# Performance work log

Hardware: AMD Instinct MI355X
Metric: run time of the kernel (lower is better)

The kernel has to match this reference:

```python
import jax, jax.numpy as jnp
import numpy as np

B, R, A, L, P = 1024, 512, 196, 2, 4  # batch, rnn_size, att_size, num_layers, num_parallels


def setup_inputs() -> dict:
    key = jax.random.key(0)
    ks = jax.random.split(key, 24)
    s = 0.02
    inp = {
        'x': jax.random.normal(ks[0], (B, R), jnp.float32),
        'att': jax.random.normal(ks[1], (B, A, R), jnp.float32),
        'inputs': jax.random.normal(ks[2], (2 * L, B, R), jnp.float32),
        # first attention block
        'Wa2a': jax.random.normal(ks[3], (A, R), jnp.float32) * s,
        'ba2a': jnp.zeros((A,), jnp.float32),
        'Wh2a': jax.random.normal(ks[4], (A, R), jnp.float32) * s,
        'bh2a': jnp.zeros((A,), jnp.float32),
        'Wd2d': jax.random.normal(ks[5], (1, A), jnp.float32) * s,
        'bd2d': jnp.zeros((1,), jnp.float32),
        # second attention block
        'Wa2a1': jax.random.normal(ks[6], (A, R), jnp.float32) * s,
        'ba2a1': jnp.zeros((A,), jnp.float32),
        'Wh2a1': jax.random.normal(ks[7], (A, R), jnp.float32) * s,
        'bh2a1': jnp.zeros((A,), jnp.float32),
        'Wd2d1': jax.random.normal(ks[8], (1, A), jnp.float32) * s,
        'bd2d1': jnp.zeros((1,), jnp.float32),
        # per-parallel LSTM gate linears, stacked over P
        'Wi2h': jax.random.normal(ks[9], (P, 4 * R, R), jnp.float32) * s,
        'bi2h': jnp.zeros((P, 4 * R), jnp.float32),
        'Wh2h': jax.random.normal(ks[10], (P, 4 * R, R), jnp.float32) * s,
        'bh2h': jnp.zeros((P, 4 * R), jnp.float32),
        'Wa2h': jax.random.normal(ks[11], (P, 4 * R, R), jnp.float32) * s,
        'ba2h': jnp.zeros((P, 4 * R), jnp.float32),
    }
    return inp


def _attend(att, h, Wa, ba, Wh, bh, Wd, bd):
    # att: [B, S, R] with S == A (code requires it); h: [B, R]
    av = jnp.einsum('bsr,ar->bsa', att, Wa) + ba            # [B, S, A]
    ah = h @ Wh.T + bh                                      # [B, A]
    # original expands h-projection along the LAST axis (unsqueeze(2).expand)
    dot = jnp.tanh(av + ah[:, :, None])                     # [B, S, A]
    score = jnp.einsum('bsa,a->bs', dot, Wd[0]) + bd[0]     # [B, S]
    w = jax.nn.softmax(score, axis=-1)
    return jnp.einsum('bsr,bs->br', att, w)                 # [B, R]


def reference(x, att, inputs, Wa2a, ba2a, Wh2a, bh2a, Wd2d, bd2d,
              Wa2a1, ba2a1, Wh2a1, bh2a1, Wd2d1, bd2d1,
              Wi2h, bi2h, Wh2h, bh2h, Wa2h, ba2h):
    R_ = x.shape[-1]
    L_ = inputs.shape[0] // 2
    outputs = []
    for i in range(L_):
        prev_c = inputs[2 * i]
        prev_h = inputs[2 * i + 1]
        xt = x if i == 0 else x + outputs[-1]
        att_res = _attend(att, prev_h, Wa2a, ba2a, Wh2a, bh2a, Wd2d, bd2d)
        # stacked per-parallel gate sums: [P, B, 4R]
        sums = (jnp.einsum('bd,pgd->pbg', xt, Wi2h) + bi2h[:, None, :]
                + jnp.einsum('bd,pgd->pbg', prev_h, Wh2h) + bh2h[:, None, :]
                + jnp.einsum('bd,pgd->pbg', att_res, Wa2h) + ba2h[:, None, :])
        ig = jax.nn.sigmoid(sums[..., :R_])
        fg = jax.nn.sigmoid(sums[..., R_:2 * R_])
        og = jax.nn.sigmoid(sums[..., 2 * R_:3 * R_])
        it = jnp.tanh(sums[..., 3 * R_:])
        nc = fg * prev_c[None] + ig * it                    # [P, B, R]
        next_c = nc.mean(axis=0)
        next_h = (og * jnp.tanh(nc)).mean(axis=0)
        att_res1 = _attend(att, next_h, Wa2a1, ba2a1, Wh2a1, bh2a1, Wd2d1, bd2d1)
        top_h = att_res1 + next_h
        outputs.append(next_c)
        outputs.append(top_h)
    return jnp.stack(outputs)  # [2L, B, R]
```

## Files before the change

kernel.cpp:

```cpp
#include <hip/hip_runtime.h>
#include <math.h>

typedef __attribute__((ext_vector_type(8))) unsigned short ushort8_t;
typedef __attribute__((ext_vector_type(8))) short bf16x8;
typedef __attribute__((ext_vector_type(4))) float f32x4;

namespace {

constexpr int Bn = 1024;
constexpr int Rn = 512;
constexpr int An = 196;
constexpr int Gn = 8192;
constexpr int Kcat = 1536;
constexpr int NP = 224;
constexpr long ROWS = (long)Bn * An;

__device__ __forceinline__ float b2f(unsigned short u) {
  union { unsigned int i; float f; } v; v.i = ((unsigned int)u) << 16; return v.f;
}
__device__ __forceinline__ unsigned short f2b(float f) {
  union { float f; unsigned int i; } v; v.f = f;
  unsigned int r = v.i + 0x7fffu + ((v.i >> 16) & 1u);
  return (unsigned short)(r >> 16);
}
__device__ __forceinline__ float sigmf(float x) {
  return __builtin_amdgcn_rcpf(1.f + __expf(-x));
}
__device__ __forceinline__ float tanhf_fast(float x) {
  const float e = __expf(2.f * x);
  return 1.f - 2.f * __builtin_amdgcn_rcpf(e + 1.f);
}

__global__ __launch_bounds__(256)
void f2b_copy(const float* __restrict__ src, unsigned short* __restrict__ dst, long n)
{
  long i = ((long)blockIdx.x * 256 + threadIdx.x) * 8;
  const long stride = (long)gridDim.x * 256 * 8;
  for (; i + 8 <= n; i += stride) {
    float4 a = *(const float4*)(src + i);
    float4 b = *(const float4*)(src + i + 4);
    ushort8_t o;
    o[0] = f2b(a.x); o[1] = f2b(a.y); o[2] = f2b(a.z); o[3] = f2b(a.w);
    o[4] = f2b(b.x); o[5] = f2b(b.y); o[6] = f2b(b.z); o[7] = f2b(b.w);
    *(ushort8_t*)(dst + i) = o;
  }
}

__global__ __launch_bounds__(256)
void pack_wpad(const float* __restrict__ Wa0, const float* __restrict__ Wa1,
               unsigned short* __restrict__ Wp)
{
  long i = ((long)blockIdx.x * 256 + threadIdx.x) * 8;
  if (i >= 2L * NP * 512) return;
  const int set = (int)(i / (NP * 512));
  const int rem = (int)(i % (NP * 512));
  const int row = rem / 512, k = rem % 512;
  ushort8_t o;
  if (row < An) {
    const float* s = (set ? Wa1 : Wa0) + (long)row * 512 + k;
    float4 a = *(const float4*)s, b = *(const float4*)(s + 4);
    o[0] = f2b(a.x); o[1] = f2b(a.y); o[2] = f2b(a.z); o[3] = f2b(a.w);
    o[4] = f2b(b.x); o[5] = f2b(b.y); o[6] = f2b(b.z); o[7] = f2b(b.w);
  } else {
    o = ushort8_t{0,0,0,0,0,0,0,0};
  }
  *(ushort8_t*)(Wp + i) = o;
}

__global__ __launch_bounds__(256)
void pack_w(const float* __restrict__ Wi, const float* __restrict__ Wh,
            const float* __restrict__ Wa, unsigned short* __restrict__ W2)
{
  long i = ((long)blockIdx.x * 256 + threadIdx.x) * 8;
  if (i >= (long)Gn * Kcat) return;
  const int g = (int)(i / Kcat);
  const int k = (int)(i % Kcat);
  const float* src = (k < 512) ? Wi + (long)g * 512 + k
                   : (k < 1024) ? Wh + (long)g * 512 + (k - 512)
                   : Wa + (long)g * 512 + (k - 1024);
  float4 a = *(const float4*)src;
  float4 b = *(const float4*)(src + 4);
  ushort8_t o;
  o[0] = f2b(a.x); o[1] = f2b(a.y); o[2] = f2b(a.z); o[3] = f2b(a.w);
  o[4] = f2b(b.x); o[5] = f2b(b.y); o[6] = f2b(b.z); o[7] = f2b(b.w);
  *(ushort8_t*)(W2 + i) = o;
}

__global__ __launch_bounds__(256)
void pack_x(const float* __restrict__ xa, const float* __restrict__ xb,
            const float* __restrict__ h, const float* __restrict__ a,
            unsigned short* __restrict__ X2)
{
  long i = ((long)blockIdx.x * 256 + threadIdx.x) * 8;
  if (i >= (long)Bn * Kcat) return;
  const int b = (int)(i / Kcat);
  const int k = (int)(i % Kcat);
  ushort8_t o;
  if (k < 512) {
    const float* s = xa + (long)b * 512 + k;
    float4 v0 = *(const float4*)s, v1 = *(const float4*)(s + 4);
    if (xb) {
      const float* s2 = xb + (long)b * 512 + k;
      float4 w0 = *(const float4*)s2, w1 = *(const float4*)(s2 + 4);
      v0.x += w0.x; v0.y += w0.y; v0.z += w0.z; v0.w += w0.w;
      v1.x += w1.x; v1.y += w1.y; v1.z += w1.z; v1.w += w1.w;
    }
    o[0] = f2b(v0.x); o[1] = f2b(v0.y); o[2] = f2b(v0.z); o[3] = f2b(v0.w);
    o[4] = f2b(v1.x); o[5] = f2b(v1.y); o[6] = f2b(v1.z); o[7] = f2b(v1.w);
  } else {
    const float* s = (k < 1024) ? h + (long)b * 512 + (k - 512)
                                : a + (long)b * 512 + (k - 1024);
    float4 v0 = *(const float4*)s, v1 = *(const float4*)(s + 4);
    o[0] = f2b(v0.x); o[1] = f2b(v0.y); o[2] = f2b(v0.z); o[3] = f2b(v0.w);
    o[4] = f2b(v1.x); o[5] = f2b(v1.y); o[6] = f2b(v1.z); o[7] = f2b(v1.w);
  }
  *(ushort8_t*)(X2 + i) = o;
}

__global__ __launch_bounds__(512, 4)
void av_cs(const unsigned short* __restrict__ A,
           const unsigned short* __restrict__ Wpad,
           const float* __restrict__ b0vec, const float* __restrict__ b1vec,
           const float* __restrict__ Wd,
           const float* __restrict__ ah0, const float* __restrict__ ah1,
           float* __restrict__ s0, float* __restrict__ s1,
           unsigned short* __restrict__ av_out)
{
  __shared__ unsigned short As[128 * 32];
  __shared__ unsigned short Bs[224 * 32];
  __shared__ float wds[NP], bas[NP];
  __shared__ float ahAs[128], ahBs[128];
  __shared__ float sbA[128], sbB[128];

  const int tid = threadIdx.x;
  const int lane = tid & 63, w = tid >> 6;
  const int wr = w >> 1, wc = w & 1;
  const int fr = lane & 15, q = lane >> 4;
  const long row0 = (long)blockIdx.x * 128;
  const int set = blockIdx.y;

  if (set == 0) {
    if (tid < NP) {
      wds[tid] = (tid < An) ? Wd[tid] : 0.f;
      bas[tid] = (tid < An) ? b0vec[tid] : 0.f;
    }
    if (tid >= 256 && tid < 384) ahAs[tid - 256] = ah0[row0 + tid - 256];
    if (tid >= 384)              ahBs[tid - 384] = ah1[row0 + tid - 384];
  } else {
    if (tid < NP) bas[tid] = (tid < An) ? b1vec[tid] : 0.f;
  }

  const unsigned short* Ab = A + row0 * 512;
  const unsigned short* Bb = Wpad + (long)set * NP * 512;

  f32x4 acc[2][7] = {};

  const int grow = lane >> 2;
  const int gchk = (lane & 3) * 8;

  for (int kt = 0; kt < 512; kt += 32) {
    {
      const unsigned short* src = Ab + (long)(w * 16 + grow) * 512 + gchk + kt;
      __builtin_amdgcn_global_load_lds(
          (const __attribute__((address_space(1))) unsigned int*)src,
          (__attribute__((address_space(3))) unsigned int*)(As + w * 512), 16, 0, 0);
    }
    {
      const unsigned short* src = Bb + (long)(w * 16 + grow) * 512 + gchk + kt;
      __builtin_amdgcn_global_load_lds(
          (const __attribute__((address_space(1))) unsigned int*)src,
          (__attribute__((address_space(3))) unsigned int*)(Bs + w * 512), 16, 0, 0);
    }
    if (w < 6) {
      const unsigned short* src = Bb + (long)((w + 8) * 16 + grow) * 512 + gchk + kt;
      __builtin_amdgcn_global_load_lds(
          (const __attribute__((address_space(1))) unsigned int*)src,
          (__attribute__((address_space(3))) unsigned int*)(Bs + (w + 8) * 512), 16, 0, 0);
    }
    __syncthreads();
    bf16x8 af[2], bfr[7];
#pragma unroll
    for (int m = 0; m < 2; ++m)
      af[m] = *(const bf16x8*)&As[(wr * 32 + m * 16 + fr) * 32 + q * 8];
#pragma unroll
    for (int n = 0; n < 7; ++n)
      bfr[n] = *(const bf16x8*)&Bs[(wc * 112 + n * 16 + fr) * 32 + q * 8];
#pragma unroll
    for (int m = 0; m < 2; ++m)
#pragma unroll
      for (int n = 0; n < 7; ++n)
        acc[m][n] = __builtin_amdgcn_mfma_f32_16x16x32_bf16(af[m], bfr[n], acc[m][n], 0, 0, 0);
    __syncthreads();
  }

  if (set == 0) {
    float pA[2][4], pB[2][4];
#pragma unroll
    for (int m = 0; m < 2; ++m)
#pragma unroll
      for (int j = 0; j < 4; ++j) { pA[m][j] = 0.f; pB[m][j] = 0.f; }
#pragma unroll
    for (int n = 0; n < 7; ++n) {
      const int col = wc * 112 + n * 16 + fr;
      const float wd = wds[col];
      const float bv = bas[col];
#pragma unroll
      for (int m = 0; m < 2; ++m) {
#pragma unroll
        for (int j = 0; j < 4; ++j) {
          const int rl = wr * 32 + m * 16 + q * 4 + j;
          const float av = acc[m][n][j] + bv;
          pA[m][j] += wd * tanhf_fast(av + ahAs[rl]);
          pB[m][j] += wd * tanhf_fast(av + ahBs[rl]);
        }
      }
    }
#pragma unroll
    for (int m = 0; m < 2; ++m)
#pragma unroll
      for (int j = 0; j < 4; ++j) {
#pragma unroll
        for (int off = 1; off < 16; off <<= 1) {
          pA[m][j] += __shfl_xor(pA[m][j], off);
          pB[m][j] += __shfl_xor(pB[m][j], off);
        }
      }
    __syncthreads();
    if (wc == 0 && fr == 0) {
#pragma unroll
      for (int m = 0; m < 2; ++m)
#pragma unroll
        for (int j = 0; j < 4; ++j) {
          const int rl = wr * 32 + m * 16 + q * 4 + j;
          sbA[rl] = pA[m][j]; sbB[rl] = pB[m][j];
        }
    }
    __syncthreads();
    if (wc == 1 && fr == 0) {
#pragma unroll
      for (int m = 0; m < 2; ++m)
#pragma unroll
        for (int j = 0; j < 4; ++j) {
          const int rl = wr * 32 + m * 16 + q * 4 + j;
          sbA[rl] += pA[m][j]; sbB[rl] += pB[m][j];
        }
    }
    __syncthreads();
    if (tid < 128) {
      s0[row0 + tid] = sbA[tid];
      s1[row0 + tid] = sbB[tid];
    }
  } else {
#pragma unroll
    for (int n = 0; n < 7; ++n) {
      const int col = wc * 112 + n * 16 + fr;
      if (col >= An) continue;
      const float bv = bas[col];
#pragma unroll
      for (int m = 0; m < 2; ++m) {
#pragma unroll
        for (int j = 0; j < 4; ++j) {
          const long row = row0 + wr * 32 + m * 16 + q * 4 + j;
          av_out[row * An + col] = f2b(acc[m][n][j] + bv);
        }
      }
    }
  }
}

__global__ __launch_bounds__(256)
void gemm_gate(const unsigned short* __restrict__ A, const unsigned short* __restrict__ Bm,
               const float* __restrict__ bias, float* __restrict__ C)
{
  __shared__ unsigned short As[128 * 32];
  __shared__ unsigned short Bs[128 * 32];
  const int tid = threadIdx.x;
  const int lane = tid & 63, w = tid >> 6;
  int bid = blockIdx.x;
  bid = (bid & 7) * (gridDim.x >> 3) + (bid >> 3);
  const int bx = bid & 63;
  const int by = bid >> 6;
  const long row0 = (long)by * 128;
  const long col0 = (long)bx * 128;
  const int wr = w >> 1, wc = w & 1;
  const int fr = lane & 15, q = lane >> 4;
  const int srow = lane >> 2, schk = lane & 3;

  f32x4 acc[4][4] = {};
  const unsigned short* A0 = A + row0 * Kcat + schk * 8;
  const unsigned short* B0 = Bm + col0 * Kcat + schk * 8;

  for (int kt = 0; kt < Kcat; kt += 32) {
#pragma unroll
    for (int i = 0; i < 2; ++i) {
      const int rr = (w * 2 + i) * 16 + srow;
      __builtin_amdgcn_global_load_lds(
          (const __attribute__((address_space(1))) unsigned int*)(A0 + (long)rr * Kcat + kt),
          (__attribute__((address_space(3))) unsigned int*)(As + (w * 2 + i) * 512),
          16, 0, 0);
      __builtin_amdgcn_global_load_lds(
          (const __attribute__((address_space(1))) unsigned int*)(B0 + (long)rr * Kcat + kt),
          (__attribute__((address_space(3))) unsigned int*)(Bs + (w * 2 + i) * 512),
          16, 0, 0);
    }
    __syncthreads();
    bf16x8 af[4], bfr[4];
#pragma unroll
    for (int m = 0; m < 4; ++m)
      af[m] = *(const bf16x8*)&As[(wr * 64 + m * 16 + fr) * 32 + q * 8];
#pragma unroll
    for (int n = 0; n < 4; ++n)
      bfr[n] = *(const bf16x8*)&Bs[(wc * 64 + n * 16 + fr) * 32 + q * 8];
#pragma unroll
    for (int m = 0; m < 4; ++m)
#pragma unroll
      for (int n = 0; n < 4; ++n)
        acc[m][n] = __builtin_amdgcn_mfma_f32_16x16x32_bf16(af[m], bfr[n], acc[m][n], 0, 0, 0);
    __syncthreads();
  }

  const int crow = wr * 64 + q * 4;
  const int ccol = wc * 64 + fr;
#pragma unroll
  for (int n = 0; n < 4; ++n) {
    const int col = (int)col0 + ccol + n * 16;
    const float bv = bias[col];
#pragma unroll
    for (int m = 0; m < 4; ++m) {
      const long rb = row0 + crow + m * 16;
#pragma unroll
      for (int j = 0; j < 4; ++j)
        C[(rb + j) * (long)Gn + col] = acc[m][n][j] + bv;
    }
  }
}

__global__ __launch_bounds__(256)
void gemm_bf(const unsigned short* __restrict__ A, const unsigned short* __restrict__ Bm,
             const float* __restrict__ bias, float* __restrict__ C,
             int N, int K, int ldc)
{
  constexpr int LDP = 56;
  __shared__ unsigned short As[128 * LDP];
  __shared__ unsigned short Bs[128 * LDP];
  const int tid = threadIdx.x;
  const long row0 = (long)blockIdx.y * 128;
  const int col0 = blockIdx.x * 128;
  const int wid = tid >> 6, lane = tid & 63;
  const int wr = wid >> 1, wc = wid & 1;
  const int fr = lane & 15, kg = (lane >> 4) * 8;

  f32x4 acc[4][4] = {};

  const int srow = tid >> 1;
  const int skh = tid & 1;
  const unsigned short* Ap = A + (row0 + srow) * (long)K + skh * 16;
  const int bcol = col0 + srow;
  const unsigned short* Bp = Bm + (long)(bcol < N ? bcol : N - 1) * K + skh * 16;

  ushort8_t a0 = *(const ushort8_t*)(Ap);
  ushort8_t a1 = *(const ushort8_t*)(Ap + 8);
  ushort8_t b0 = *(const ushort8_t*)(Bp);
  ushort8_t b1 = *(const ushort8_t*)(Bp + 8);

  const int sw = srow * LDP + skh * 16;
  for (int kt = 0; kt < K; kt += 32) {
    *(ushort8_t*)&As[sw] = a0;
    *(ushort8_t*)&As[sw + 8] = a1;
    *(ushort8_t*)&Bs[sw] = b0;
    *(ushort8_t*)&Bs[sw + 8] = b1;
    if (kt + 32 < K) {
      a0 = *(const ushort8_t*)(Ap + kt + 32);
      a1 = *(const ushort8_t*)(Ap + kt + 40);
      b0 = *(const ushort8_t*)(Bp + kt + 32);
      b1 = *(const ushort8_t*)(Bp + kt + 40);
    }
    __syncthreads();
    bf16x8 af[4], bfr[4];
#pragma unroll
    for (int m = 0; m < 4; ++m)
      af[m] = *(const bf16x8*)&As[(wr * 64 + m * 16 + fr) * LDP + kg];
#pragma unroll
    for (int n = 0; n < 4; ++n)
      bfr[n] = *(const bf16x8*)&Bs[(wc * 64 + n * 16 + fr) * LDP + kg];
#pragma unroll
    for (int m = 0; m < 4; ++m)
#pragma unroll
      for (int n = 0; n < 4; ++n)
        acc[m][n] = __builtin_amdgcn_mfma_f32_16x16x32_bf16(af[m], bfr[n], acc[m][n], 0, 0, 0);
    __syncthreads();
  }

  const int crow = wr * 64 + (lane >> 4) * 4;
  const int ccol = wc * 64 + fr;
#pragma unroll
  for (int n = 0; n < 4; ++n) {
    const int col = col0 + ccol + n * 16;
    if (col >= N) continue;
    const float bv = bias ? bias[col] : 0.f;
#pragma unroll
    for (int m = 0; m < 4; ++m) {
      const long rb = row0 + crow + m * 16;
#pragma unroll
      for (int j = 0; j < 4; ++j)
        C[(rb + j) * (long)ldc + col] = acc[m][n][j] + bv;
    }
  }
}

__global__ __launch_bounds__(256)
void score1(const unsigned short* __restrict__ av, const float* __restrict__ ah,
            const float* __restrict__ Wd, float* __restrict__ s0)
{
  const int row = blockIdx.x * 4 + (threadIdx.x >> 6);
  const int lane = threadIdx.x & 63;
  const unsigned short* avp = av + (long)row * An;
  const float A0 = ah[row];
  float v0 = 0.f;
  for (int a = lane; a < An; a += 64)
    v0 += Wd[a] * tanhf_fast(b2f(avp[a]) + A0);
#pragma unroll
  for (int o = 32; o; o >>= 1) v0 += __shfl_down(v0, o);
  if (lane == 0) s0[row] = v0;
}

template<bool DUAL>
__global__ __launch_bounds__(256)
void wsum2(const unsigned short* __restrict__ att,
           const float* __restrict__ w0, const float* __restrict__ w1,
           const float* __restrict__ add0,
           float* __restrict__ o0, float* __restrict__ o1)
{
  const int half = threadIdx.x >> 7;
  const int b = blockIdx.x * 2 + half;
  const int t = threadIdx.x & 127;
  const int wv = t >> 6;
  __shared__ float ws0[2][An], ws1[2][An];
  __shared__ float redm[2][2][2], redsum[2][2][2];

  const float r0a = w0[(long)b * An + t];
  const float r0b = (t + 128 < An) ? w0[(long)b * An + t + 128] : -3.0e38f;
  float r1a = -3.0e38f, r1b = -3.0e38f;
  if (DUAL) {
    r1a = w1[(long)b * An + t];
    r1b = (t + 128 < An) ? w1[(long)b * An + t + 128] : -3.0e38f;
  }
  float m0 = fmaxf(r0a, r0b), m1 = fmaxf(r1a, r1b);
#pragma unroll
  for (int o = 32; o; o >>= 1) {
    m0 = fmaxf(m0, __shfl_xor(m0, o));
    if (DUAL) m1 = fmaxf(m1, __shfl_xor(m1, o));
  }
  if ((t & 63) == 0) { redm[0][half][wv] = m0; if (DUAL) redm[1][half][wv] = m1; }
  __syncthreads();
  m0 = fmaxf(redm[0][half][0], redm[0][half][1]);
  if (DUAL) m1 = fmaxf(redm[1][half][0], redm[1][half][1]);
  const float e0a = __expf(r0a - m0);
  const float e0b = (t + 128 < An) ? __expf(r0b - m0) : 0.f;
  float sl0 = e0a + e0b, sl1 = 0.f;
  float e1a = 0.f, e1b = 0.f;
  if (DUAL) {
    e1a = __expf(r1a - m1);
    e1b = (t + 128 < An) ? __expf(r1b - m1) : 0.f;
    sl1 = e1a + e1b;
  }
#pragma unroll
  for (int o = 32; o; o >>= 1) {
    sl0 += __shfl_xor(sl0, o);
    if (DUAL) sl1 += __shfl_xor(sl1, o);
  }
  if ((t & 63) == 0) { redsum[0][half][wv] = sl0; if (DUAL) redsum[1][half][wv] = sl1; }
  __syncthreads();
  const float inv0 = __builtin_amdgcn_rcpf(redsum[0][half][0] + redsum[0][half][1]);
  ws0[half][t] = e0a * inv0;
  if (t + 128 < An) ws0[half][t + 128] = e0b * inv0;
  if (DUAL) {
    const float inv1 = __builtin_amdgcn_rcpf(redsum[1][half][0] + redsum[1][half][1]);
    ws1[half][t] = e1a * inv1;
    if (t + 128 < An) ws1[half][t + 128] = e1b * inv1;
  }
  __syncthreads();

  const unsigned short* ap = att + (long)b * An * Rn + t * 4;
  float a00 = 0, a01 = 0, a02 = 0, a03 = 0;
  float a10 = 0, a11 = 0, a12 = 0, a13 = 0;
  for (int s = 0; s < An; ++s) {
    ushort4 u = *(const ushort4*)(ap + (long)s * Rn);
    const float f0 = b2f(u.x), f1 = b2f(u.y), f2 = b2f(u.z), f3 = b2f(u.w);
    const float v0 = ws0[half][s];
    a00 = fmaf(f0, v0, a00); a01 = fmaf(f1, v0, a01);
    a02 = fmaf(f2, v0, a02); a03 = fmaf(f3, v0, a03);
    if (DUAL) {
      const float v1 = ws1[half][s];
      a10 = fmaf(f0, v1, a10); a11 = fmaf(f1, v1, a11);
      a12 = fmaf(f2, v1, a12); a13 = fmaf(f3, v1, a13);
    }
  }
  const long base = (long)b * Rn + t * 4;
  if (add0) {
    float4 ad = *(const float4*)(add0 + base);
    a00 += ad.x; a01 += ad.y; a02 += ad.z; a03 += ad.w;
  }
  *(float4*)(o0 + base) = make_float4(a00, a01, a02, a03);
  if (DUAL) *(float4*)(o1 + base) = make_float4(a10, a11, a12, a13);
}

__global__ __launch_bounds__(256)
void gates_pw(const float* __restrict__ sums, const float* __restrict__ prev_c,
              float* __restrict__ out_c, float* __restrict__ nh,
              unsigned short* __restrict__ nh_bf)
{
  const int i = blockIdx.x * 256 + threadIdx.x;
  const int b = i >> 9;
  const int r = i & 511;
  const float c = prev_c[i];
  float aC = 0.f, aH = 0.f;
#pragma unroll
  for (int p = 0; p < 4; ++p) {
    const float* sp = sums + (long)b * Gn + p * 2048 + r;
    const float ig = sigmf(sp[0]);
    const float fg = sigmf(sp[512]);
    const float og = sigmf(sp[1024]);
    const float it = tanhf_fast(sp[1536]);
    const float nc = fmaf(fg, c, ig * it);
    aC += nc;
    aH = fmaf(og, tanhf_fast(nc), aH);
  }
  out_c[i] = aC * 0.25f;
  const float hv = aH * 0.25f;
  nh[i] = hv;
  nh_bf[i] = f2b(hv);
}

__global__ __launch_bounds__(256)
void bias3(const float* __restrict__ a, const float* __restrict__ b,
           const float* __restrict__ c, float* __restrict__ o, int n)
{
  const int i = blockIdx.x * 256 + threadIdx.x;
  if (i < n) o[i] = a[i] + b[i] + c[i];
}

}

extern "C" void kernel_launch(void* const* d_in, const int* in_sizes, int n_in,
                              void* d_out, int out_size, void* d_ws, size_t ws_size,
                              hipStream_t stream)
{
  const float* x      = (const float*)d_in[0];
  const float* att    = (const float*)d_in[1];
  const float* inputs = (const float*)d_in[2];
  const float* Wa2a   = (const float*)d_in[3];
  const float* ba2a   = (const float*)d_in[4];
  const float* Wh2a   = (const float*)d_in[5];
  const float* bh2a   = (const float*)d_in[6];
  const float* Wd2d   = (const float*)d_in[7];
  const float* Wa2a1  = (const float*)d_in[9];
  const float* ba2a1  = (const float*)d_in[10];
  const float* Wh2a1  = (const float*)d_in[11];
  const float* bh2a1  = (const float*)d_in[12];
  const float* Wd2d1  = (const float*)d_in[13];
  const float* Wi2h   = (const float*)d_in[15];
  const float* bi2h   = (const float*)d_in[16];
  const float* Wh2h   = (const float*)d_in[17];
  const float* bh2h   = (const float*)d_in[18];
  const float* Wa2h   = (const float*)d_in[19];
  const float* ba2h   = (const float*)d_in[20];
  (void)in_sizes; (void)n_in; (void)out_size; (void)ws_size;

  float* out = (float*)d_out;
  const float* prev_c0 = inputs + 0 * (long)Bn * Rn;
  const float* prev_h0 = inputs + 1 * (long)Bn * Rn;
  const float* prev_c1 = inputs + 2 * (long)Bn * Rn;
  const float* prev_h1 = inputs + 3 * (long)Bn * Rn;

  char* wsp = (char*)d_ws;
  size_t off = 0;
  auto alloc = [&](size_t bytes) -> void* {
    void* p = wsp + off;
    off += (bytes + 1023) & ~(size_t)1023;
    return p;
  };
  unsigned short* att_bf  = (unsigned short*)alloc(ROWS * Rn * 2);
  unsigned short* W2      = (unsigned short*)alloc((size_t)Gn * Kcat * 2);
  unsigned short* Wpad    = (unsigned short*)alloc((size_t)2 * NP * Rn * 2);
  unsigned short* wh2a_bf = (unsigned short*)alloc((size_t)An * Rn * 2);
  unsigned short* wh2a1_bf= (unsigned short*)alloc((size_t)An * Rn * 2);
  unsigned short* h01_bf  = (unsigned short*)alloc((size_t)2 * Bn * Rn * 2);
  unsigned short* nh_bf   = (unsigned short*)alloc((size_t)Bn * Rn * 2);
  unsigned short* X2      = (unsigned short*)alloc((size_t)Bn * Kcat * 2);
  unsigned short* av1_bf  = (unsigned short*)alloc(ROWS * An * 2);
  float* ahAB = (float*)alloc((size_t)2 * ROWS * 4);
  float* ah1  = (float*)alloc(ROWS * 4);
  float* scA  = (float*)alloc(ROWS * 4);
  float* scB  = (float*)alloc(ROWS * 4);
  float* sc1  = (float*)alloc(ROWS * 4);
  float* res0 = (float*)alloc((size_t)Bn * Rn * 4);
  float* res1 = (float*)alloc((size_t)Bn * Rn * 4);
  float* nh   = (float*)alloc((size_t)Bn * Rn * 4);
  float* bsum = (float*)alloc((size_t)Gn * 4);
  float* sums = (float*)alloc((size_t)Bn * Gn * 4);

  float* ahA = ahAB;
  float* ahB = ahAB + ROWS;

  const dim3 blk(256);

  f2b_copy<<<dim3(50176), blk, 0, stream>>>(att, att_bf, ROWS * Rn);
  pack_wpad<<<dim3(112), blk, 0, stream>>>(Wa2a, Wa2a1, Wpad);
  f2b_copy<<<dim3(49), blk, 0, stream>>>(Wh2a,  wh2a_bf,  (long)An * Rn);
  f2b_copy<<<dim3(49), blk, 0, stream>>>(Wh2a1, wh2a1_bf, (long)An * Rn);
  f2b_copy<<<dim3(256), blk, 0, stream>>>(prev_h0, h01_bf, (long)Bn * Rn);
  f2b_copy<<<dim3(256), blk, 0, stream>>>(prev_h1, h01_bf + (long)Bn * Rn, (long)Bn * Rn);
  pack_w<<<dim3(6144), blk, 0, stream>>>(Wi2h, Wh2h, Wa2h, W2);
  bias3<<<dim3(Gn / 256), blk, 0, stream>>>(bi2h, bh2h, ba2h, bsum, Gn);

  gemm_bf<<<dim3(2, 16), blk, 0, stream>>>(h01_bf, wh2a_bf, bh2a, ahA, An, Rn, An);

  av_cs<<<dim3((int)(ROWS / 128), 2), dim3(512), 0, stream>>>(
      att_bf, Wpad, ba2a, ba2a1, Wd2d, ahA, ahB, scA, scB, av1_bf);
  wsum2<true><<<dim3(Bn / 2), blk, 0, stream>>>(att_bf, scA, scB, (const float*)nullptr, res0, res1);

  pack_x<<<dim3(768), blk, 0, stream>>>(x, (const float*)nullptr, prev_h0, res0, X2);
  gemm_gate<<<dim3(512), blk, 0, stream>>>(X2, W2, bsum, sums);
  gates_pw<<<dim3(Bn * Rn / 256), blk, 0, stream>>>(sums, prev_c0, out + 0, nh, nh_bf);

  gemm_bf<<<dim3(2, Bn / 128), blk, 0, stream>>>(nh_bf, wh2a1_bf, bh2a1, ah1, An, Rn, An);
  score1<<<dim3((int)(ROWS / 4)), blk, 0, stream>>>(av1_bf, ah1, Wd2d1, sc1);
  wsum2<false><<<dim3(Bn / 2), blk, 0, stream>>>(att_bf, sc1, (const float*)nullptr, nh,
                                                 out + (long)Bn * Rn, (float*)nullptr);

  pack_x<<<dim3(768), blk, 0, stream>>>(x, out + (long)Bn * Rn, prev_h1, res1, X2);
  gemm_gate<<<dim3(512), blk, 0, stream>>>(X2, W2, bsum, sums);
  gates_pw<<<dim3(Bn * Rn / 256), blk, 0, stream>>>(sums, prev_c1, out + 2 * (long)Bn * Rn, nh, nh_bf);

  gemm_bf<<<dim3(2, Bn / 128), blk, 0, stream>>>(nh_bf, wh2a1_bf, bh2a1, ah1, An, Rn, An);
  score1<<<dim3((int)(ROWS / 4)), blk, 0, stream>>>(av1_bf, ah1, Wd2d1, sc1);
  wsum2<false><<<dim3(Bn / 2), blk, 0, stream>>>(att_bf, sc1, (const float*)nullptr, nh,
                                                 out + 3 * (long)Bn * Rn, (float*)nullptr);
}
```

Baseline: 714.5 us.

## Fuse attention scoring, softmax, weighted sum and gate-input packing per batch row

Replaces score1+wsum2+pack_x with fused per-batch kernels: attend1 writes both first-block attention results straight into two pre-packed bf16 gate-input buffers, and attend2 stages the av1 slab in shared memory, computes scores, softmax and weighted sum, and writes the output plus the next layer's x input. The x/h sections of both gate inputs are packed once upfront, and the small conversion launches are merged. This removes several launches and intermediate fp32 round trips. The cost is a large shared-memory slab (about 77KB) in attend2, which limits occupancy, and the score loop there uses only 196 of 256 threads with serial per-thread tanh work.

```diff
diff --git a/kernel.cpp b/kernel.cpp
--- a/kernel.cpp
+++ b/kernel.cpp
@@ -68,6 +68,35 @@
 }
 
 __global__ __launch_bounds__(256)
+void pack_wh(const float* __restrict__ a, const float* __restrict__ b,
+             unsigned short* __restrict__ dst)
+{
+  long i = ((long)blockIdx.x * 256 + threadIdx.x) * 8;
+  if (i >= 2L * An * 512) return;
+  const long half = (long)An * 512;
+  const float* s = (i < half) ? a + i : b + (i - half);
+  float4 v0 = *(const float4*)s, v1 = *(const float4*)(s + 4);
+  ushort8_t o;
+  o[0] = f2b(v0.x); o[1] = f2b(v0.y); o[2] = f2b(v0.z); o[3] = f2b(v0.w);
+  o[4] = f2b(v1.x); o[5] = f2b(v1.y); o[6] = f2b(v1.z); o[7] = f2b(v1.w);
+  *(ushort8_t*)(dst + i) = o;
+}
+
+__global__ __launch_bounds__(256)
+void pack_h01(const float* __restrict__ inputs, unsigned short* __restrict__ dst)
+{
+  long i = ((long)blockIdx.x * 256 + threadIdx.x) * 8;
+  if (i >= 2L * Bn * 512) return;
+  const long half = (long)Bn * 512;
+  const float* s = (i < half) ? inputs + half + i : inputs + 3 * half + (i - half);
+  float4 v0 = *(const float4*)s, v1 = *(const float4*)(s + 4);
+  ushort8_t o;
+  o[0] = f2b(v0.x); o[1] = f2b(v0.y); o[2] = f2b(v0.z); o[3] = f2b(v0.w);
+  o[4] = f2b(v1.x); o[5] = f2b(v1.y); o[6] = f2b(v1.z); o[7] = f2b(v1.w);
+  *(ushort8_t*)(dst + i) = o;
+}
+
+__global__ __launch_bounds__(256)
 void pack_w(const float* __restrict__ Wi, const float* __restrict__ Wh,
             const float* __restrict__ Wa, unsigned short* __restrict__ W2)
 {
@@ -87,34 +116,23 @@
 }
 
 __global__ __launch_bounds__(256)
-void pack_x(const float* __restrict__ xa, const float* __restrict__ xb,
-            const float* __restrict__ h, const float* __restrict__ a,
-            unsigned short* __restrict__ X2)
+void pack_sec3(const float* __restrict__ x, const float* __restrict__ h0,
+               const float* __restrict__ h1,
+               unsigned short* __restrict__ X20, unsigned short* __restrict__ X21)
 {
   long i = ((long)blockIdx.x * 256 + threadIdx.x) * 8;
-  if (i >= (long)Bn * Kcat) return;
-  const int b = (int)(i / Kcat);
-  const int k = (int)(i % Kcat);
+  if (i >= 3L * Bn * 512) return;
+  const int sec = (int)(i / ((long)Bn * 512));
+  const long r = i % ((long)Bn * 512);
+  const int b = (int)(r >> 9);
+  const int k = (int)(r & 511);
+  const float* src = (sec == 0 ? x : sec == 1 ? h0 : h1) + r;
+  unsigned short* dst = (sec == 2 ? X21 : X20) + (long)b * Kcat + (sec ? 512 : 0) + k;
+  float4 v0 = *(const float4*)src, v1 = *(const float4*)(src + 4);
   ushort8_t o;
-  if (k < 512) {
-    const float* s = xa + (long)b * 512 + k;
-    float4 v0 = *(const float4*)s, v1 = *(const float4*)(s + 4);
-    if (xb) {
-      const float* s2 = xb + (long)b * 512 + k;
-      float4 w0 = *(const float4*)s2, w1 = *(const float4*)(s2 + 4);
-      v0.x += w0.x; v0.y += w0.y; v0.z += w0.z; v0.w += w0.w;
-      v1.x += w1.x; v1.y += w1.y; v1.z += w1.z; v1.w += w1.w;
-    }
-    o[0] = f2b(v0.x); o[1] = f2b(v0.y); o[2] = f2b(v0.z); o[3] = f2b(v0.w);
-    o[4] = f2b(v1.x); o[5] = f2b(v1.y); o[6] = f2b(v1.z); o[7] = f2b(v1.w);
-  } else {
-    const float* s = (k < 1024) ? h + (long)b * 512 + (k - 512)
-                                : a + (long)b * 512 + (k - 1024);
-    float4 v0 = *(const float4*)s, v1 = *(const float4*)(s + 4);
-    o[0] = f2b(v0.x); o[1] = f2b(v0.y); o[2] = f2b(v0.z); o[3] = f2b(v0.w);
-    o[4] = f2b(v1.x); o[5] = f2b(v1.y); o[6] = f2b(v1.z); o[7] = f2b(v1.w);
-  }
-  *(ushort8_t*)(X2 + i) = o;
+  o[0] = f2b(v0.x); o[1] = f2b(v0.y); o[2] = f2b(v0.z); o[3] = f2b(v0.w);
+  o[4] = f2b(v1.x); o[5] = f2b(v1.y); o[6] = f2b(v1.z); o[7] = f2b(v1.w);
+  *(ushort8_t*)dst = o;
 }
 
 __global__ __launch_bounds__(512, 4)
@@ -409,100 +427,154 @@
 }
 
 __global__ __launch_bounds__(256)
-void score1(const unsigned short* __restrict__ av, const float* __restrict__ ah,
-            const float* __restrict__ Wd, float* __restrict__ s0)
-{
-  const int row = blockIdx.x * 4 + (threadIdx.x >> 6);
-  const int lane = threadIdx.x & 63;
-  const unsigned short* avp = av + (long)row * An;
-  const float A0 = ah[row];
-  float v0 = 0.f;
-  for (int a = lane; a < An; a += 64)
-    v0 += Wd[a] * tanhf_fast(b2f(avp[a]) + A0);
-#pragma unroll
-  for (int o = 32; o; o >>= 1) v0 += __shfl_down(v0, o);
-  if (lane == 0) s0[row] = v0;
-}
-
-template<bool DUAL>
-__global__ __launch_bounds__(256)
-void wsum2(const unsigned short* __restrict__ att,
-           const float* __restrict__ w0, const float* __restrict__ w1,
-           const float* __restrict__ add0,
-           float* __restrict__ o0, float* __restrict__ o1)
-{
-  const int half = threadIdx.x >> 7;
-  const int b = blockIdx.x * 2 + half;
-  const int t = threadIdx.x & 127;
-  const int wv = t >> 6;
-  __shared__ float ws0[2][An], ws1[2][An];
-  __shared__ float redm[2][2][2], redsum[2][2][2];
-
-  const float r0a = w0[(long)b * An + t];
-  const float r0b = (t + 128 < An) ? w0[(long)b * An + t + 128] : -3.0e38f;
-  float r1a = -3.0e38f, r1b = -3.0e38f;
-  if (DUAL) {
-    r1a = w1[(long)b * An + t];
-    r1b = (t + 128 < An) ? w1[(long)b * An + t + 128] : -3.0e38f;
-  }
-  float m0 = fmaxf(r0a, r0b), m1 = fmaxf(r1a, r1b);
+void attend1(const unsigned short* __restrict__ att,
+             const float* __restrict__ scA, const float* __restrict__ scB,
+             unsigned short* __restrict__ X20, unsigned short* __restrict__ X21)
+{
+  __shared__ float wsA[An], wsB[An];
+  __shared__ float red[2][4];
+  __shared__ float part[128][8];
+  const int b = blockIdx.x, tid = threadIdx.x, wv = tid >> 6;
+
+  float vA = -3.0e38f, vB = -3.0e38f;
+  if (tid < An) { vA = scA[(long)b * An + tid]; vB = scB[(long)b * An + tid]; }
+  float mA = vA, mB = vB;
 #pragma unroll
   for (int o = 32; o; o >>= 1) {
-    m0 = fmaxf(m0, __shfl_xor(m0, o));
-    if (DUAL) m1 = fmaxf(m1, __shfl_xor(m1, o));
-  }
-  if ((t & 63) == 0) { redm[0][half][wv] = m0; if (DUAL) redm[1][half][wv] = m1; }
-  __syncthreads();
-  m0 = fmaxf(redm[0][half][0], redm[0][half][1]);
-  if (DUAL) m1 = fmaxf(redm[1][half][0], redm[1][half][1]);
-  const float e0a = __expf(r0a - m0);
-  const float e0b = (t + 128 < An) ? __expf(r0b - m0) : 0.f;
-  float sl0 = e0a + e0b, sl1 = 0.f;
-  float e1a = 0.f, e1b = 0.f;
-  if (DUAL) {
-    e1a = __expf(r1a - m1);
-    e1b = (t + 128 < An) ? __expf(r1b - m1) : 0.f;
-    sl1 = e1a + e1b;
-  }
-#pragma unroll
-  for (int o = 32; o; o >>= 1) {
-    sl0 += __shfl_xor(sl0, o);
-    if (DUAL) sl1 += __shfl_xor(sl1, o);
-  }
-  if ((t & 63) == 0) { redsum[0][half][wv] = sl0; if (DUAL) redsum[1][half][wv] = sl1; }
-  __syncthreads();
-  const float inv0 = __builtin_amdgcn_rcpf(redsum[0][half][0] + redsum[0][half][1]);
-  ws0[half][t] = e0a * inv0;
-  if (t + 128 < An) ws0[half][t + 128] = e0b * inv0;
-  if (DUAL) {
-    const float inv1 = __builtin_amdgcn_rcpf(redsum[1][half][0] + redsum[1][half][1]);
-    ws1[half][t] = e1a * inv1;
-    if (t + 128 < An) ws1[half][t + 128] = e1b * inv1;
-  }
-  __syncthreads();
-
+    mA = fmaxf(mA, __shfl_xor(mA, o));
+    mB = fmaxf(mB, __shfl_xor(mB, o));
+  }
+  if ((tid & 63) == 0) { red[0][wv] = mA; red[1][wv] = mB; }
+  __syncthreads();
+  mA = fmaxf(fmaxf(red[0][0], red[0][1]), fmaxf(red[0][2], red[0][3]));
+  mB = fmaxf(fmaxf(red[1][0], red[1][1]), fmaxf(red[1][2], red[1][3]));
+  const float eA = (tid < An) ? __expf(vA - mA) : 0.f;
+  const float eB = (tid < An) ? __expf(vB - mB) : 0.f;
+  float sA = eA, sB = eB;
+#pragma unroll
+  for (int o = 32; o; o >>= 1) { sA += __shfl_xor(sA, o); sB += __shfl_xor(sB, o); }
+  __syncthreads();
+  if ((tid & 63) == 0) { red[0][wv] = sA; red[1][wv] = sB; }
+  __syncthreads();
+  sA = red[0][0] + red[0][1] + red[0][2] + red[0][3];
+  sB = red[1][0] + red[1][1] + red[1][2] + red[1][3];
+  if (tid < An) {
+    wsA[tid] = eA * __builtin_amdgcn_rcpf(sA);
+    wsB[tid] = eB * __builtin_amdgcn_rcpf(sB);
+  }
+  __syncthreads();
+
+  const int half = tid >> 7, t = tid & 127;
+  float aA[4] = {0, 0, 0, 0}, aB[4] = {0, 0, 0, 0};
+  const int sS = half * 98, sE = half ? An : 98;
   const unsigned short* ap = att + (long)b * An * Rn + t * 4;
-  float a00 = 0, a01 = 0, a02 = 0, a03 = 0;
-  float a10 = 0, a11 = 0, a12 = 0, a13 = 0;
-  for (int s = 0; s < An; ++s) {
+  for (int s = sS; s < sE; ++s) {
     ushort4 u = *(const ushort4*)(ap + (long)s * Rn);
     const float f0 = b2f(u.x), f1 = b2f(u.y), f2 = b2f(u.z), f3 = b2f(u.w);
-    const float v0 = ws0[half][s];
-    a00 = fmaf(f0, v0, a00); a01 = fmaf(f1, v0, a01);
-    a02 = fmaf(f2, v0, a02); a03 = fmaf(f3, v0, a03);
-    if (DUAL) {
-      const float v1 = ws1[half][s];
-      a10 = fmaf(f0, v1, a10); a11 = fmaf(f1, v1, a11);
-      a12 = fmaf(f2, v1, a12); a13 = fmaf(f3, v1, a13);
-    }
-  }
-  const long base = (long)b * Rn + t * 4;
-  if (add0) {
-    float4 ad = *(const float4*)(add0 + base);
-    a00 += ad.x; a01 += ad.y; a02 += ad.z; a03 += ad.w;
-  }
-  *(float4*)(o0 + base) = make_float4(a00, a01, a02, a03);
-  if (DUAL) *(float4*)(o1 + base) = make_float4(a10, a11, a12, a13);
+    const float wA = wsA[s], wB = wsB[s];
+    aA[0] = fmaf(f0, wA, aA[0]); aA[1] = fmaf(f1, wA, aA[1]);
+    aA[2] = fmaf(f2, wA, aA[2]); aA[3] = fmaf(f3, wA, aA[3]);
+    aB[0] = fmaf(f0, wB, aB[0]); aB[1] = fmaf(f1, wB, aB[1]);
+    aB[2] = fmaf(f2, wB, aB[2]); aB[3] = fmaf(f3, wB, aB[3]);
+  }
+  if (half) {
+#pragma unroll
+    for (int j = 0; j < 4; ++j) { part[t][j] = aA[j]; part[t][4 + j] = aB[j]; }
+  }
+  __syncthreads();
+  if (!half) {
+    ushort4 oA, oB;
+    oA.x = f2b(aA[0] + part[t][0]); oA.y = f2b(aA[1] + part[t][1]);
+    oA.z = f2b(aA[2] + part[t][2]); oA.w = f2b(aA[3] + part[t][3]);
+    oB.x = f2b(aB[0] + part[t][4]); oB.y = f2b(aB[1] + part[t][5]);
+    oB.z = f2b(aB[2] + part[t][6]); oB.w = f2b(aB[3] + part[t][7]);
+    *(ushort4*)(X20 + (long)b * Kcat + 1024 + t * 4) = oA;
+    *(ushort4*)(X21 + (long)b * Kcat + 1024 + t * 4) = oB;
+  }
+}
+
+template<bool WX2>
+__global__ __launch_bounds__(256)
+void attend2(const unsigned short* __restrict__ av1,
+             const float* __restrict__ ah,
+             const float* __restrict__ Wd,
+             const unsigned short* __restrict__ att,
+             const float* __restrict__ addv,
+             const float* __restrict__ xin,
+             float* __restrict__ oout,
+             unsigned short* __restrict__ X2)
+{
+  __shared__ unsigned short slab[An * An];
+  __shared__ float wds[An];
+  __shared__ float ws[An];
+  __shared__ float red[4];
+  const int b = blockIdx.x, tid = threadIdx.x, wv = tid >> 6;
+
+  if (tid < An) wds[tid] = Wd[tid];
+  {
+    const ushort4* src = (const ushort4*)(av1 + (long)b * An * An);
+    ushort4* dl = (ushort4*)slab;
+    for (int i = tid; i < (An * An) / 4; i += 256) dl[i] = src[i];
+  }
+  __syncthreads();
+
+  float sc = -3.0e38f;
+  if (tid < An) {
+    const float A0 = ah[(long)b * An + tid];
+    const unsigned short* rp = slab + tid * An;
+    float v = 0.f;
+    for (int a = 0; a < An; ++a) v += wds[a] * tanhf_fast(b2f(rp[a]) + A0);
+    sc = v;
+  }
+  float m = sc;
+#pragma unroll
+  for (int o = 32; o; o >>= 1) m = fmaxf(m, __shfl_xor(m, o));
+  if ((tid & 63) == 0) red[wv] = m;
+  __syncthreads();
+  m = fmaxf(fmaxf(red[0], red[1]), fmaxf(red[2], red[3]));
+  const float e = (tid < An) ? __expf(sc - m) : 0.f;
+  float s = e;
+#pragma unroll
+  for (int o = 32; o; o >>= 1) s += __shfl_xor(s, o);
+  __syncthreads();
+  if ((tid & 63) == 0) red[wv] = s;
+  __syncthreads();
+  s = red[0] + red[1] + red[2] + red[3];
+  if (tid < An) ws[tid] = e * __builtin_amdgcn_rcpf(s);
+  __syncthreads();
+
+  const int half = tid >> 7, t = tid & 127;
+  float a0 = 0, a1 = 0, a2 = 0, a3 = 0;
+  const int sS = half * 98, sE = half ? An : 98;
+  const unsigned short* ap = att + (long)b * An * Rn + t * 4;
+  for (int si = sS; si < sE; ++si) {
+    ushort4 u = *(const ushort4*)(ap + (long)si * Rn);
+    const float w = ws[si];
+    a0 = fmaf(b2f(u.x), w, a0); a1 = fmaf(b2f(u.y), w, a1);
+    a2 = fmaf(b2f(u.z), w, a2); a3 = fmaf(b2f(u.w), w, a3);
+  }
+  float* part = (float*)slab;
+  __syncthreads();
+  if (half) {
+    part[t * 4 + 0] = a0; part[t * 4 + 1] = a1;
+    part[t * 4 + 2] = a2; part[t * 4 + 3] = a3;
+  }
+  __syncthreads();
+  if (!half) {
+    a0 += part[t * 4 + 0]; a1 += part[t * 4 + 1];
+    a2 += part[t * 4 + 2]; a3 += part[t * 4 + 3];
+    const long base = (long)b * Rn + t * 4;
+    float4 ad = *(const float4*)(addv + base);
+    a0 += ad.x; a1 += ad.y; a2 += ad.z; a3 += ad.w;
+    *(float4*)(oout + base) = make_float4(a0, a1, a2, a3);
+    if (WX2) {
+      float4 xv = *(const float4*)(xin + base);
+      ushort4 o;
+      o.x = f2b(a0 + xv.x); o.y = f2b(a1 + xv.y);
+      o.z = f2b(a2 + xv.z); o.w = f2b(a3 + xv.w);
+      *(ushort4*)(X2 + (long)b * Kcat + t * 4) = o;
+    }
+  }
 }
 
 __global__ __launch_bounds__(256)
@@ -583,58 +655,55 @@
   unsigned short* att_bf  = (unsigned short*)alloc(ROWS * Rn * 2);
   unsigned short* W2      = (unsigned short*)alloc((size_t)Gn * Kcat * 2);
   unsigned short* Wpad    = (unsigned short*)alloc((size_t)2 * NP * Rn * 2);
-  unsigned short* wh2a_bf = (unsigned short*)alloc((size_t)An * Rn * 2);
-  unsigned short* wh2a1_bf= (unsigned short*)alloc((size_t)An * Rn * 2);
+  unsigned short* whcat   = (unsigned short*)alloc((size_t)2 * An * Rn * 2);
   unsigned short* h01_bf  = (unsigned short*)alloc((size_t)2 * Bn * Rn * 2);
   unsigned short* nh_bf   = (unsigned short*)alloc((size_t)Bn * Rn * 2);
-  unsigned short* X2      = (unsigned short*)alloc((size_t)Bn * Kcat * 2);
+  unsigned short* X20     = (unsigned short*)alloc((size_t)Bn * Kcat * 2);
+  unsigned short* X21     = (unsigned short*)alloc((size_t)Bn * Kcat * 2);
   unsigned short* av1_bf  = (unsigned short*)alloc(ROWS * An * 2);
   float* ahAB = (float*)alloc((size_t)2 * ROWS * 4);
   float* ah1  = (float*)alloc(ROWS * 4);
   float* scA  = (float*)alloc(ROWS * 4);
   float* scB  = (float*)alloc(ROWS * 4);
-  float* sc1  = (float*)alloc(ROWS * 4);
-  float* res0 = (float*)alloc((size_t)Bn * Rn * 4);
-  float* res1 = (float*)alloc((size_t)Bn * Rn * 4);
   float* nh   = (float*)alloc((size_t)Bn * Rn * 4);
   float* bsum = (float*)alloc((size_t)Gn * 4);
   float* sums = (float*)alloc((size_t)Bn * Gn * 4);
 
   float* ahA = ahAB;
   float* ahB = ahAB + ROWS;
+  unsigned short* wh2a_bf  = whcat;
+  unsigned short* wh2a1_bf = whcat + (size_t)An * Rn;
 
   const dim3 blk(256);
 
   f2b_copy<<<dim3(50176), blk, 0, stream>>>(att, att_bf, ROWS * Rn);
   pack_wpad<<<dim3(112), blk, 0, stream>>>(Wa2a, Wa2a1, Wpad);
-  f2b_copy<<<dim3(49), blk, 0, stream>>>(Wh2a,  wh2a_bf,  (long)An * Rn);
-  f2b_copy<<<dim3(49), blk, 0, stream>>>(Wh2a1, wh2a1_bf, (long)An * Rn);
-  f2b_copy<<<dim3(256), blk, 0, stream>>>(prev_h0, h01_bf, (long)Bn * Rn);
-  f2b_copy<<<dim3(256), blk, 0, stream>>>(prev_h1, h01_bf + (long)Bn * Rn, (long)Bn * Rn);
+  pack_wh<<<dim3(98), blk, 0, stream>>>(Wh2a, Wh2a1, whcat);
+  pack_h01<<<dim3(512), blk, 0, stream>>>(inputs, h01_bf);
   pack_w<<<dim3(6144), blk, 0, stream>>>(Wi2h, Wh2h, Wa2h, W2);
   bias3<<<dim3(Gn / 256), blk, 0, stream>>>(bi2h, bh2h, ba2h, bsum, Gn);
+  pack_sec3<<<dim3(768), blk, 0, stream>>>(x, prev_h0, prev_h1, X20, X21);
 
   gemm_bf<<<dim3(2, 16), blk, 0, stream>>>(h01_bf, wh2a_bf, bh2a, ahA, An, Rn, An);
 
   av_cs<<<dim3((int)(ROWS / 128), 2), dim3(512), 0, stream>>>(
       att_bf, Wpad, ba2a, ba2a1, Wd2d, ahA, ahB, scA, scB, av1_bf);
-  wsum2<true><<<dim3(Bn / 2), blk, 0, stream>>>(att_bf, scA, scB, (const float*)nullptr, res0, res1);
-
-  pack_x<<<dim3(768), blk, 0, stream>>>(x, (const float*)nullptr, prev_h0, res0, X2);
-  gemm_gate<<<dim3(512), blk, 0, stream>>>(X2, W2, bsum, sums);
+
+  attend1<<<dim3(Bn), blk, 0, stream>>>(att_bf, scA, scB, X20, X21);
+
+  gemm_gate<<<dim3(512), blk, 0, stream>>>(X20, W2, bsum, sums);
   gates_pw<<<dim3(Bn * Rn / 256), blk, 0, stream>>>(sums, prev_c0, out + 0, nh, nh_bf);
 
   gemm_bf<<<dim3(2, Bn / 128), blk, 0, stream>>>(nh_bf, wh2a1_bf, bh2a1, ah1, An, Rn, An);
-  score1<<<dim3((int)(ROWS / 4)), blk, 0, stream>>>(av1_bf, ah1, Wd2d1, sc1);
-  wsum2<false><<<dim3(Bn / 2), blk, 0, stream>>>(att_bf, sc1, (const float*)nullptr, nh,
-                                                 out + (long)Bn * Rn, (float*)nullptr);
-
-  pack_x<<<dim3(768), blk, 0, stream>>>(x, out + (long)Bn * Rn, prev_h1, res1, X2);
-  gemm_gate<<<dim3(512), blk, 0, stream>>>(X2, W2, bsum, sums);
+  attend2<true><<<dim3(Bn), blk, 0, stream>>>(av1_bf, ah1, Wd2d1, att_bf, nh, x,
+                                              out + (long)Bn * Rn, X21);
+
+  gemm_gate<<<dim3(512), blk, 0, stream>>>(X21, W2, bsum, sums);
   gates_pw<<<dim3(Bn * Rn / 256), blk, 0, stream>>>(sums, prev_c1, out + 2 * (long)Bn * Rn, nh, nh_bf);
 
   gemm_bf<<<dim3(2, Bn / 128), blk, 0, stream>>>(nh_bf, wh2a1_bf, bh2a1, ah1, An, Rn, An);
-  score1<<<dim3((int)(ROWS / 4)), blk, 0, stream>>>(av1_bf, ah1, Wd2d1, sc1);
-  wsum2<false><<<dim3(Bn / 2), blk, 0, stream>>>(att_bf, sc1, (const float*)nullptr, nh,
-                                                 out + 3 * (long)Bn * Rn, (float*)nullptr);
-}
+  attend2<false><<<dim3(Bn), blk, 0, stream>>>(av1_bf, ah1, Wd2d1, att_bf, nh,
+                                               (const float*)nullptr,
+                                               out + 3 * (long)Bn * Rn,
+                                               (unsigned short*)nullptr);
+}
```

New measurement: 822.9 us. 15.2% more time.
